# Optimization experiments

Measured on AMD Instinct MI355X. Metric: run time of the kernel, lower is better.

Reference implementation:

```python
import jax, jax.numpy as jnp
import numpy as np

N_FINE = 200000
N_COARSE = 50000
NNZ = 400000
F = 128


def setup_inputs() -> dict:
    key = jax.random.key(0)
    k1, k2, k3, k4 = jax.random.split(key, 4)
    x_fine = jax.random.normal(k1, (N_FINE, F), dtype=jnp.float32)
    r_vals = jax.random.uniform(k2, (NNZ,), dtype=jnp.float32)
    r_rows = jax.random.randint(k3, (NNZ,), 0, N_COARSE, dtype=jnp.int64)
    r_cols = jax.random.randint(k4, (NNZ,), 0, N_FINE, dtype=jnp.int64)
    return {"x_fine": x_fine, "r_vals": r_vals, "r_rows": r_rows, "r_cols": r_cols}


def reference(x_fine, r_vals, r_rows, r_cols):
    # h_coarse = R @ x_fine, R in COO format (rows, cols, vals), shape [N_c, N_f].
    # Gather fine-node features at nonzero columns, weight, and segment-sum by row.
    gathered = x_fine[r_cols] * r_vals[:, None]          # [nnz, F]
    h_coarse = jax.ops.segment_sum(gathered, r_rows, num_segments=N_COARSE)  # [N_c, F]
    return h_coarse
```

## Files before the change

kernel.cpp:

```cpp
#include <hip/hip_runtime.h>
#include <hip/hip_bf16.h>


#define F   128
#define CAP 16

__global__ __launch_bounds__(256) void scatter_bins(
    const int*   __restrict__ rows, const int* __restrict__ cols,
    const float* __restrict__ vals,
    int* __restrict__ counts, int2* __restrict__ bins,
    int* __restrict__ ovf_cnt, int3* __restrict__ ovf, int nnz)
{
    int i = blockIdx.x * blockDim.x + threadIdx.x;
    if (i >= nnz) return;
    int   r = __builtin_nontemporal_load(rows + i);
    int   c = __builtin_nontemporal_load(cols + i);
    float v = __builtin_nontemporal_load(vals + i);
    int pos = atomicAdd(&counts[r], 1);
    if (pos < CAP) {
        bins[(size_t)r * CAP + pos] = make_int2(c, __float_as_int(v));
    } else {
        int p = atomicAdd(ovf_cnt, 1);
        ovf[p] = make_int3(r, c, __float_as_int(v));
    }
}

__global__ __launch_bounds__(256) void gather_rows(
    const float* __restrict__ x_fine, const int2* __restrict__ bins,
    const int* __restrict__ counts, float* __restrict__ out, int n_rows)
{
    int gid  = blockIdx.x * blockDim.x + threadIdx.x;
    int row  = gid >> 6;
    int lane = gid & 63;
    if (row >= n_rows) return;

    int deg = counts[row];
    if (deg > CAP) deg = CAP;

    int2 e = make_int2(0, 0);
    if (lane < deg) e = bins[(size_t)row * CAP + lane];

    const float2* xf = reinterpret_cast<const float2*>(x_fine);
    float2 acc = make_float2(0.f, 0.f);
    int deg8 = (deg + 7) & ~7;

    for (int j = 0; j < deg8; j += 8) {
        int   cc[8];
        float ww[8];
#pragma unroll
        for (int k = 0; k < 8; ++k) {
            cc[k] = __shfl(e.x, j + k);
            ww[k] = __int_as_float(__shfl(e.y, j + k));
        }
        float2 vv[8];
#pragma unroll
        for (int k = 0; k < 8; ++k)
            vv[k] = xf[(size_t)cc[k] * 64 + lane];
#pragma unroll
        for (int k = 0; k < 8; ++k) {
            acc.x += ww[k] * vv[k].x;
            acc.y += ww[k] * vv[k].y;
        }
    }
    reinterpret_cast<float2*>(out)[(size_t)row * 64 + lane] = acc;
}

__global__ __launch_bounds__(256) void ovf_apply(
    const float* __restrict__ x_fine, const int3* __restrict__ ovf,
    const int* __restrict__ ovf_cnt, float* __restrict__ out)
{
    int n = *ovf_cnt;
    int total = n * 32;
    for (int idx = blockIdx.x * blockDim.x + threadIdx.x; idx < total;
         idx += gridDim.x * blockDim.x) {
        int e = idx >> 5, q = idx & 31;
        int3 t = ovf[e];
        float val = __int_as_float(t.z);
        float4 v = reinterpret_cast<const float4*>(x_fine + (size_t)t.y * F)[q];
        float* o = out + (size_t)t.x * F + q * 4;
        unsafeAtomicAdd(o + 0, v.x * val);
        unsafeAtomicAdd(o + 1, v.y * val);
        unsafeAtomicAdd(o + 2, v.z * val);
        unsafeAtomicAdd(o + 3, v.w * val);
    }
}

extern "C" void kernel_launch(void* const* d_in, const int* in_sizes, int n_in,
                              void* d_out, int out_size, void* d_ws, size_t ws_size,
                              hipStream_t stream) {
    const float* x_fine = (const float*)d_in[0];
    const float* r_vals = (const float*)d_in[1];
    const int*   r_rows = (const int*)d_in[2];
    const int*   r_cols = (const int*)d_in[3];
    float* out = (float*)d_out;

    int nnz    = in_sizes[1];
    int n_rows = out_size / F;

    size_t counts_b = (size_t)n_rows * 4;
    size_t ovf_b    = (size_t)nnz * 12;
    size_t fixed    = counts_b + 16 + ovf_b;

    char* ws = (char*)d_ws;
    int*  counts  = (int*)ws;
    int*  ovf_cnt = (int*)(ws + counts_b);
    int3* ovf     = (int3*)(ws + counts_b + 16);
    int2* bins    = (int2*)(ws + fixed);

    hipMemsetAsync(counts, 0, counts_b + 16, stream);

    int b_nnz = (nnz + 255) / 256;
    hipLaunchKernelGGL(scatter_bins, dim3(b_nnz), dim3(256), 0, stream,
                       r_rows, r_cols, r_vals, counts, bins,
                       ovf_cnt, ovf, nnz);

    int b_rows = (int)(((size_t)n_rows * 64 + 255) / 256);
    hipLaunchKernelGGL(gather_rows, dim3(b_rows), dim3(256), 0, stream,
                       x_fine, bins, counts, out, n_rows);

    hipLaunchKernelGGL(ovf_apply, dim3(64), dim3(256), 0, stream,
                       x_fine, ovf, ovf_cnt, out);
}
```

Before: 202.5 us.

## Fuse memset, binning, gather and overflow into one cooperative persistent kernel

Replaces the memset and three separate kernel launches with a single cooperative kernel of 1024 persistent blocks, using grid-wide syncs between the zeroing, scatter-to-bins, per-row gather and overflow phases. The goal is to remove launch overhead and inter-kernel gaps. In exchange it pays for three grid barriers and limits parallelism to a fixed grid that loops over rows, which may lower occupancy and latency hiding in the gather phase.

```diff
diff --git a/kernel.cpp b/kernel.cpp
--- a/kernel.cpp
+++ b/kernel.cpp
@@ -1,80 +1,88 @@
 #include <hip/hip_runtime.h>
-#include <hip/hip_bf16.h>
+#include <hip/hip_cooperative_groups.h>
+
+namespace cg = cooperative_groups;
 
 
-#define F   128
-#define CAP 16
+#define F    128
+#define CAP  16
+#define NBLK 1024
+#define NTHR 256
 
-__global__ __launch_bounds__(256) void scatter_bins(
-    const int*   __restrict__ rows, const int* __restrict__ cols,
-    const float* __restrict__ vals,
-    int* __restrict__ counts, int2* __restrict__ bins,
-    int* __restrict__ ovf_cnt, int3* __restrict__ ovf, int nnz)
+__global__ __launch_bounds__(NTHR) void fused_restrict(
+    const float* __restrict__ x_fine,
+    const float* __restrict__ r_vals,
+    const int*   __restrict__ r_rows,
+    const int*   __restrict__ r_cols,
+    float*       __restrict__ out,
+    int*         __restrict__ counts,
+    int2*        __restrict__ bins,
+    int*         __restrict__ ovf_cnt,
+    int3*        __restrict__ ovf,
+    int nnz, int n_rows)
 {
-    int i = blockIdx.x * blockDim.x + threadIdx.x;
-    if (i >= nnz) return;
-    int   r = __builtin_nontemporal_load(rows + i);
-    int   c = __builtin_nontemporal_load(cols + i);
-    float v = __builtin_nontemporal_load(vals + i);
-    int pos = atomicAdd(&counts[r], 1);
-    if (pos < CAP) {
-        bins[(size_t)r * CAP + pos] = make_int2(c, __float_as_int(v));
-    } else {
-        int p = atomicAdd(ovf_cnt, 1);
-        ovf[p] = make_int3(r, c, __float_as_int(v));
-    }
-}
+    cg::grid_group grid = cg::this_grid();
+    const int tid = blockIdx.x * NTHR + threadIdx.x;
+    const int nth = NBLK * NTHR;
 
-__global__ __launch_bounds__(256) void gather_rows(
-    const float* __restrict__ x_fine, const int2* __restrict__ bins,
-    const int* __restrict__ counts, float* __restrict__ out, int n_rows)
-{
-    int gid  = blockIdx.x * blockDim.x + threadIdx.x;
-    int row  = gid >> 6;
-    int lane = gid & 63;
-    if (row >= n_rows) return;
+    for (int i = tid; i < n_rows; i += nth) counts[i] = 0;
+    if (tid == 0) *ovf_cnt = 0;
+    grid.sync();
 
-    int deg = counts[row];
-    if (deg > CAP) deg = CAP;
-
-    int2 e = make_int2(0, 0);
-    if (lane < deg) e = bins[(size_t)row * CAP + lane];
-
-    const float2* xf = reinterpret_cast<const float2*>(x_fine);
-    float2 acc = make_float2(0.f, 0.f);
-    int deg8 = (deg + 7) & ~7;
-
-    for (int j = 0; j < deg8; j += 8) {
-        int   cc[8];
-        float ww[8];
-#pragma unroll
-        for (int k = 0; k < 8; ++k) {
-            cc[k] = __shfl(e.x, j + k);
-            ww[k] = __int_as_float(__shfl(e.y, j + k));
-        }
-        float2 vv[8];
-#pragma unroll
-        for (int k = 0; k < 8; ++k)
-            vv[k] = xf[(size_t)cc[k] * 64 + lane];
-#pragma unroll
-        for (int k = 0; k < 8; ++k) {
-            acc.x += ww[k] * vv[k].x;
-            acc.y += ww[k] * vv[k].y;
+    for (int i = tid; i < nnz; i += nth) {
+        int   r = __builtin_nontemporal_load(r_rows + i);
+        int   c = __builtin_nontemporal_load(r_cols + i);
+        float v = __builtin_nontemporal_load(r_vals + i);
+        int pos = atomicAdd(&counts[r], 1);
+        if (pos < CAP) {
+            bins[(size_t)r * CAP + pos] = make_int2(c, __float_as_int(v));
+        } else {
+            int p = atomicAdd(ovf_cnt, 1);
+            ovf[p] = make_int3(r, c, __float_as_int(v));
         }
     }
-    reinterpret_cast<float2*>(out)[(size_t)row * 64 + lane] = acc;
-}
+    grid.sync();
 
-__global__ __launch_bounds__(256) void ovf_apply(
-    const float* __restrict__ x_fine, const int3* __restrict__ ovf,
-    const int* __restrict__ ovf_cnt, float* __restrict__ out)
-{
+    const int wid  = tid >> 6;
+    const int lane = tid & 63;
+    const int nwaves = nth >> 6;
+    const float2* xf = reinterpret_cast<const float2*>(x_fine);
+    for (int row = wid; row < n_rows; row += nwaves) {
+        int deg = counts[row];
+        if (deg > CAP) deg = CAP;
+
+        int2 e = make_int2(0, 0);
+        if (lane < deg) e = bins[(size_t)row * CAP + lane];
+
+        float2 acc = make_float2(0.f, 0.f);
+        int deg8 = (deg + 7) & ~7;
+        for (int j = 0; j < deg8; j += 8) {
+            int   cc[8];
+            float ww[8];
+#pragma unroll
+            for (int k = 0; k < 8; ++k) {
+                cc[k] = __shfl(e.x, j + k);
+                ww[k] = __int_as_float(__shfl(e.y, j + k));
+            }
+            float2 vv[8];
+#pragma unroll
+            for (int k = 0; k < 8; ++k)
+                vv[k] = xf[(size_t)cc[k] * 64 + lane];
+#pragma unroll
+            for (int k = 0; k < 8; ++k) {
+                acc.x += ww[k] * vv[k].x;
+                acc.y += ww[k] * vv[k].y;
+            }
+        }
+        reinterpret_cast<float2*>(out)[(size_t)row * 64 + lane] = acc;
+    }
+    grid.sync();
+
     int n = *ovf_cnt;
     int total = n * 32;
-    for (int idx = blockIdx.x * blockDim.x + threadIdx.x; idx < total;
-         idx += gridDim.x * blockDim.x) {
-        int e = idx >> 5, q = idx & 31;
-        int3 t = ovf[e];
+    for (int idx = tid; idx < total; idx += nth) {
+        int e32 = idx >> 5, q = idx & 31;
+        int3 t = ovf[e32];
         float val = __int_as_float(t.z);
         float4 v = reinterpret_cast<const float4*>(x_fine + (size_t)t.y * F)[q];
         float* o = out + (size_t)t.x * F + q * 4;
@@ -107,17 +115,11 @@
     int3* ovf     = (int3*)(ws + counts_b + 16);
     int2* bins    = (int2*)(ws + fixed);
 
-    hipMemsetAsync(counts, 0, counts_b + 16, stream);
-
-    int b_nnz = (nnz + 255) / 256;
-    hipLaunchKernelGGL(scatter_bins, dim3(b_nnz), dim3(256), 0, stream,
-                       r_rows, r_cols, r_vals, counts, bins,
-                       ovf_cnt, ovf, nnz);
-
-    int b_rows = (int)(((size_t)n_rows * 64 + 255) / 256);
-    hipLaunchKernelGGL(gather_rows, dim3(b_rows), dim3(256), 0, stream,
-                       x_fine, bins, counts, out, n_rows);
-
-    hipLaunchKernelGGL(ovf_apply, dim3(64), dim3(256), 0, stream,
-                       x_fine, ovf, ovf_cnt, out);
+    void* args[] = {
+        (void*)&x_fine, (void*)&r_vals, (void*)&r_rows, (void*)&r_cols,
+        (void*)&out, (void*)&counts, (void*)&bins, (void*)&ovf_cnt,
+        (void*)&ovf, (void*)&nnz, (void*)&n_rows
+    };
+    hipLaunchCooperativeKernel((const void*)fused_restrict,
+                               dim3(NBLK), dim3(NTHR), args, 0, stream);
 }
```

Result: slower. 502.1 us (+148.0%).
